# Kernel tuning notes

Hardware: AMD Instinct MI355X
Metric: run time of the kernel (lower is better)

## Reference

```python
import jax, jax.numpy as jnp
import numpy as np

GAMMA_NEG = 4.0
GAMMA_POS = 1.0
CLIP = 0.05
EPS = 1e-08
ALPHA3 = 2.0
TOPK = 10
B, C = 4096, 9605


def setup_inputs() -> dict:
    key = jax.random.key(0)
    k1, k2, k3, k4, k5, k6 = jax.random.split(key, 6)
    x = jax.random.normal(k1, (B, C), dtype=jnp.float32)
    y = (jax.random.uniform(k2, (B, C)) < 0.02).astype(jnp.float32)
    whitelist_mask = jax.random.randint(k3, (C,), 0, 100) == 0
    compost_idx = jax.random.randint(k4, (70,), 0, C, dtype=jnp.int32)
    recycle_idx = jax.random.randint(k5, (70,), 0, C, dtype=jnp.int32)
    donate_idx = jax.random.randint(k6, (70,), 0, C, dtype=jnp.int32)
    return {"x": x, "y": y, "whitelist_mask": whitelist_mask,
            "compost_idx": compost_idx, "recycle_idx": recycle_idx,
            "donate_idx": donate_idx}


def reference(x, y, whitelist_mask, compost_idx, recycle_idx, donate_idx):
    xs_pos = jax.nn.sigmoid(x)                       # [B, C]
    xs_neg = jnp.minimum(1.0 - xs_pos + CLIP, 1.0)   # asymmetric clipping
    # base binary cross-entropy (positive log term, clamped)
    loss = (y * jnp.log(jnp.maximum(xs_pos, EPS))
            + (1.0 - y) * jnp.log(jnp.maximum(xs_neg, EPS)))

    # per-sample: does ground truth hit any whitelist (compost/recycle/donate)?
    wl_idx = jnp.concatenate([compost_idx, recycle_idx, donate_idx])  # [210]
    gt_none = jnp.sum(y[:, wl_idx], axis=1) == 0.0    # [B] -> gt_whitelist == [4]

    # top-10 predictions per sample (argsort descending, first 10)
    _, top10 = jax.lax.top_k(xs_pos, TOPK)            # [B, 10]
    y_top = jnp.take_along_axis(y, top10, axis=1)     # [B, 10]
    wl_top = whitelist_mask[top10]                    # [B, 10]
    # non-whitelisted class: penalize iff gt hits no whitelist
    # whitelisted class:     penalize iff y[i, index] == 0
    penalize = jnp.where(wl_top, y_top == 0.0, gt_none[:, None])  # [B, 10]
    mult_vals = jnp.where(penalize, ALPHA3, 1.0)      # [B, 10]
    rows = jnp.arange(x.shape[0])[:, None]
    mult = jnp.ones_like(loss).at[rows, top10].set(mult_vals)
    loss = loss * mult

    # asymmetric focal weighting (no grad through the weight)
    pt = xs_pos * y + xs_neg * (1.0 - y)
    one_sided_gamma = GAMMA_POS * y + GAMMA_NEG * (1.0 - y)
    one_sided_w = jax.lax.stop_gradient(jnp.power(1.0 - pt, one_sided_gamma))
    loss = loss * one_sided_w
    return -jnp.sum(loss)
```

## Files before the change

### kernel.cpp

```cpp
#include <hip/hip_runtime.h>
#include <stdint.h>

#define B_DIM 4096
#define C_DIM 9605
#define NT 512
#define NW (NT / 64)
#define CHUNKS 4
#define VEC_N (NT * 4 * CHUNKS)
#define TOPK_N 10
#define CAP 1024
#define LOG2E_F 1.4426950408889634f
#define LN2_D 0.6931471805599453
#define CLIP_F 0.05f
#define XTHRESH 2.5f

typedef float f4a __attribute__((ext_vector_type(4), aligned(16)));

__device__ __forceinline__ float sigmoid_f(float x) {
  float e = __builtin_amdgcn_exp2f(-x * LOG2E_F);
  return __builtin_amdgcn_rcpf(1.0f + e);
}

__device__ __forceinline__ float loss2_term(float s, bool pos) {
  float xn = fminf(1.0f + CLIP_F - s, 1.0f);
  float z = pos ? s : xn;
  float logz = __builtin_amdgcn_logf(z);
  float t = fmaxf(s - CLIP_F, 0.0f);
  float t2 = t * t;
  float w = pos ? (1.0f - s) : (t2 * t2);
  return logz * w;
}

__device__ __forceinline__ unsigned long long make_key(float s, int c, bool pos) {
  return ((unsigned long long)__float_as_uint(s) << 15)
       | (unsigned long long)(((uint32_t)(c ^ 0x3FFF) << 1) | (pos ? 1u : 0u));
}

__device__ __forceinline__ void process_elem(float xval, float yval, int c,
                                             float& lsum,
                                             unsigned long long* cand, int* cnt) {
  float s = sigmoid_f(xval);
  bool pos = (yval != 0.0f);
  lsum += loss2_term(s, pos);
  if (xval > XTHRESH) {
    int slot = atomicAdd(cnt, 1);
    if (slot < CAP) cand[slot] = make_key(s, c, pos);
  }
}

__global__ __launch_bounds__(NT, 4) void asym_loss_row_kernel(
    const float* __restrict__ x, const float* __restrict__ y,
    const unsigned char* __restrict__ wl_mask,
    const int* __restrict__ compost, const int* __restrict__ recycle,
    const int* __restrict__ donate, float* __restrict__ row_out) {
  __shared__ unsigned long long cand[CAP];
  __shared__ float s_part[NW];
  __shared__ int s_cnt;
  __shared__ int s_gtany;

  const int row = blockIdx.x;
  const int tid = threadIdx.x;
  const int lane = tid & 63;
  const int wid = tid >> 6;
  const float* xr = x + (size_t)row * C_DIM;
  const float* yr = y + (size_t)row * C_DIM;

  if (tid == 0) { s_cnt = 0; s_gtany = 0; }
  __syncthreads();

  if (tid < 210) {
    int idx = (tid < 70) ? compost[tid]
            : (tid < 140) ? recycle[tid - 70]
                          : donate[tid - 140];
    if (yr[idx] != 0.0f) atomicOr(&s_gtany, 1);
  }

  const int a = (4 - (row & 3)) & 3;
  float lsum = 0.0f;
  if (tid < a) process_elem(xr[tid], yr[tid], tid, lsum, cand, &s_cnt);

  const float* xa = xr + a;
  const float* ya = yr + a;
  f4a X[CHUNKS], Y[CHUNKS];
#pragma unroll
  for (int k = 0; k < CHUNKS; ++k) {
    int c4 = (k * NT + tid) * 4;
    X[k] = *(const f4a*)(xa + c4);
    Y[k] = *(const f4a*)(ya + c4);
  }
#pragma unroll
  for (int k = 0; k < CHUNKS; ++k) {
    int c4 = a + (k * NT + tid) * 4;
#pragma unroll
    for (int j = 0; j < 4; ++j)
      process_elem(X[k][j], Y[k][j], c4 + j, lsum, cand, &s_cnt);
  }
  for (int c = a + VEC_N + tid; c < C_DIM; c += NT)
    process_elem(xr[c], yr[c], c, lsum, cand, &s_cnt);

#pragma unroll
  for (int off = 32; off; off >>= 1) lsum += __shfl_xor(lsum, off, 64);
  if (lane == 0) s_part[wid] = lsum;
  __syncthreads();

  if (wid == 0) {
    const int n = s_cnt;
    const bool gt_none = (s_gtany == 0);
    unsigned long long prev = ~0ull;
    unsigned long long mykey = 0ull;

    if (n >= TOPK_N && n <= CAP) {
#pragma unroll 1
      for (int r = 0; r < TOPK_N; ++r) {
        unsigned long long loc = 0ull;
        for (int i = lane; i < n; i += 64) {
          unsigned long long k = cand[i];
          if (k < prev && k > loc) loc = k;
        }
#pragma unroll
        for (int off = 32; off; off >>= 1) {
          unsigned long long o = __shfl_xor(loc, off, 64);
          loc = loc > o ? loc : o;
        }
        if (lane == r) mykey = loc;
        prev = loc;
      }
    } else {
#pragma unroll 1
      for (int r = 0; r < TOPK_N; ++r) {
        unsigned long long loc = 0ull;
        for (int i = lane; i < C_DIM; i += 64) {
          float s = sigmoid_f(xr[i]);
          unsigned long long k = make_key(s, i, yr[i] != 0.0f);
          if (k < prev && k > loc) loc = k;
        }
#pragma unroll
        for (int off = 32; off; off >>= 1) {
          unsigned long long o = __shfl_xor(loc, off, 64);
          loc = loc > o ? loc : o;
        }
        if (lane == r) mykey = loc;
        prev = loc;
      }
    }

    float extra = 0.0f;
    if (lane < TOPK_N) {
      int wc = 0x3FFF ^ (int)((mykey >> 1) & 0x3FFFull);
      bool ypos = (mykey & 1ull) != 0ull;
      float s = __uint_as_float((uint32_t)(mykey >> 15));
      bool wl = (wl_mask[wc] != 0);
      bool pen = wl ? (!ypos) : gt_none;
      if (pen) extra = loss2_term(s, ypos);
    }
#pragma unroll
    for (int off = 32; off; off >>= 1) extra += __shfl_xor(extra, off, 64);
    if (lane == 0) {
      float tot = extra;
#pragma unroll
      for (int w2 = 0; w2 < NW; ++w2) tot += s_part[w2];
      row_out[row] = tot;
    }
  }
}

__global__ void finalize_kernel(const float* __restrict__ row_out,
                                float* __restrict__ out) {
  const int tid = threadIdx.x;
  const int lane = tid & 63;
  const int wid = tid >> 6;
  __shared__ double sp[4];
  double acc = 0.0;
  for (int i = tid; i < B_DIM; i += 256) acc += (double)row_out[i];
#pragma unroll
  for (int off = 32; off; off >>= 1) acc += __shfl_down(acc, off, 64);
  if (lane == 0) sp[wid] = acc;
  __syncthreads();
  if (tid == 0) {
    double t = sp[0] + sp[1] + sp[2] + sp[3];
    out[0] = (float)(-t * LN2_D);
  }
}

extern "C" void kernel_launch(void* const* d_in, const int* in_sizes, int n_in,
                              void* d_out, int out_size, void* d_ws, size_t ws_size,
                              hipStream_t stream) {
  (void)in_sizes; (void)n_in; (void)out_size; (void)ws_size;
  const float* x = (const float*)d_in[0];
  const float* y = (const float*)d_in[1];
  const unsigned char* wl = (const unsigned char*)d_in[2];
  const int* compost = (const int*)d_in[3];
  const int* recycle = (const int*)d_in[4];
  const int* donate  = (const int*)d_in[5];
  float* row_part = (float*)d_ws;

  asym_loss_row_kernel<<<B_DIM, NT, 0, stream>>>(x, y, wl, compost, recycle,
                                                 donate, row_part);
  finalize_kernel<<<1, 256, 0, stream>>>(row_part, (float*)d_out);
}
```

Measured before the change: 66.15 us.

## Vectorize tail columns, hoist all loads ahead of compute, batch candidate checks

```diff
diff --git a/kernel.cpp b/kernel.cpp
--- a/kernel.cpp
+++ b/kernel.cpp
@@ -5,8 +5,6 @@
 #define C_DIM 9605
 #define NT 512
 #define NW (NT / 64)
-#define CHUNKS 4
-#define VEC_N (NT * 4 * CHUNKS)
 #define TOPK_N 10
 #define CAP 1024
 #define LOG2E_F 1.4426950408889634f
@@ -48,6 +46,27 @@
   }
 }
 
+__device__ __forceinline__ void process4(const f4a xv, const f4a yv, int cb,
+                                         bool active, float& lsum,
+                                         unsigned long long* cand, int* cnt) {
+  float sv[4], l = 0.0f;
+#pragma unroll
+  for (int j = 0; j < 4; ++j) {
+    sv[j] = sigmoid_f(xv[j]);
+    l += loss2_term(sv[j], yv[j] != 0.0f);
+  }
+  if (active) lsum += l;
+  float mx = fmaxf(fmaxf(xv[0], xv[1]), fmaxf(xv[2], xv[3]));
+  if (active && mx > XTHRESH) {
+#pragma unroll
+    for (int j = 0; j < 4; ++j)
+      if (xv[j] > XTHRESH) {
+        int slot = atomicAdd(cnt, 1);
+        if (slot < CAP) cand[slot] = make_key(sv[j], cb + j, yv[j] != 0.0f);
+      }
+  }
+}
+
 __global__ __launch_bounds__(NT, 4) void asym_loss_row_kernel(
     const float* __restrict__ x, const float* __restrict__ y,
     const unsigned char* __restrict__ wl_mask,
@@ -68,34 +87,44 @@
   if (tid == 0) { s_cnt = 0; s_gtany = 0; }
   __syncthreads();
 
+  const int a = (4 - (row & 3)) & 3;
+  const float* xa = xr + a;
+  const float* ya = yr + a;
+  const int Tend = (C_DIM - a - 4) & ~3;
+
+  float ywl = 0.0f;
   if (tid < 210) {
     int idx = (tid < 70) ? compost[tid]
             : (tid < 140) ? recycle[tid - 70]
                           : donate[tid - 140];
-    if (yr[idx] != 0.0f) atomicOr(&s_gtany, 1);
-  }
-
-  const int a = (4 - (row & 3)) & 3;
-  float lsum = 0.0f;
-  if (tid < a) process_elem(xr[tid], yr[tid], tid, lsum, cand, &s_cnt);
-
-  const float* xa = xr + a;
-  const float* ya = yr + a;
-  f4a X[CHUNKS], Y[CHUNKS];
-#pragma unroll
-  for (int k = 0; k < CHUNKS; ++k) {
+    ywl = yr[idx];
+  }
+
+  f4a X[5], Y[5];
+  int c4t = 4 * NT * 4 + 4 * tid;
+  const bool tact = (c4t <= Tend);
+  if (!tact) c4t = Tend;
+#pragma unroll
+  for (int k = 0; k < 4; ++k) {
     int c4 = (k * NT + tid) * 4;
     X[k] = *(const f4a*)(xa + c4);
     Y[k] = *(const f4a*)(ya + c4);
   }
-#pragma unroll
-  for (int k = 0; k < CHUNKS; ++k) {
-    int c4 = a + (k * NT + tid) * 4;
-#pragma unroll
-    for (int j = 0; j < 4; ++j)
-      process_elem(X[k][j], Y[k][j], c4 + j, lsum, cand, &s_cnt);
-  }
-  for (int c = a + VEC_N + tid; c < C_DIM; c += NT)
+  X[4] = *(const f4a*)(xa + c4t);
+  Y[4] = *(const f4a*)(ya + c4t);
+
+  asm volatile("" : "+v"(X[0]), "+v"(X[1]), "+v"(X[2]), "+v"(X[3]), "+v"(X[4]),
+                    "+v"(Y[0]), "+v"(Y[1]), "+v"(Y[2]), "+v"(Y[3]), "+v"(Y[4]));
+
+  if (ywl != 0.0f) atomicOr(&s_gtany, 1);
+
+  float lsum = 0.0f;
+  if (tid < a) process_elem(xr[tid], yr[tid], tid, lsum, cand, &s_cnt);
+#pragma unroll
+  for (int k = 0; k < 4; ++k)
+    process4(X[k], Y[k], a + (k * NT + tid) * 4, true, lsum, cand, &s_cnt);
+  process4(X[4], Y[4], a + c4t, tact, lsum, cand, &s_cnt);
+  for (int c = a + Tend + 4 + tid; c < C_DIM; c += NT)
     process_elem(xr[c], yr[c], c, lsum, cand, &s_cnt);
 
 #pragma unroll
```

After: 63.82 us. 3.5% less time.

## Split row kernel into flat grid-stride stream pass plus per-row top-k kernel

Applied to the files above, without the earlier changes.

```diff
diff --git a/kernel.cpp b/kernel.cpp
--- a/kernel.cpp
+++ b/kernel.cpp
@@ -3,18 +3,22 @@
 
 #define B_DIM 4096
 #define C_DIM 9605
-#define NT 512
-#define NW (NT / 64)
-#define CHUNKS 4
-#define VEC_N (NT * 4 * CHUNKS)
+#define E_TOT 39341965
+#define E_LAST 39341964
+#define QTOT 9835491
+#define NB1 2048
+#define NT1 256
 #define TOPK_N 10
-#define CAP 1024
+#define CAP 80
 #define LOG2E_F 1.4426950408889634f
 #define LN2_D 0.6931471805599453
 #define CLIP_F 0.05f
-#define XTHRESH 2.5f
+#define XTHRESH 2.65f
+#define DIV_MAGIC 114472840ull
+#define DIV_SHIFT 40
 
 typedef float f4a __attribute__((ext_vector_type(4), aligned(16)));
+typedef unsigned long long u64;
 
 __device__ __forceinline__ float sigmoid_f(float x) {
   float e = __builtin_amdgcn_exp2f(-x * LOG2E_F);
@@ -31,147 +35,157 @@
   return logz * w;
 }
 
-__device__ __forceinline__ unsigned long long make_key(float s, int c, bool pos) {
-  return ((unsigned long long)__float_as_uint(s) << 15)
-       | (unsigned long long)(((uint32_t)(c ^ 0x3FFF) << 1) | (pos ? 1u : 0u));
-}
-
-__device__ __forceinline__ void process_elem(float xval, float yval, int c,
-                                             float& lsum,
-                                             unsigned long long* cand, int* cnt) {
-  float s = sigmoid_f(xval);
-  bool pos = (yval != 0.0f);
-  lsum += loss2_term(s, pos);
-  if (xval > XTHRESH) {
-    int slot = atomicAdd(cnt, 1);
-    if (slot < CAP) cand[slot] = make_key(s, c, pos);
-  }
-}
-
-__global__ __launch_bounds__(NT, 4) void asym_loss_row_kernel(
+__device__ __forceinline__ uint32_t fmono(float v) {
+  uint32_t b = __float_as_uint(v);
+  return (b & 0x80000000u) ? ~b : (b | 0x80000000u);
+}
+__device__ __forceinline__ float fmono_dec(uint32_t m) {
+  return __uint_as_float((m & 0x80000000u) ? (m & 0x7FFFFFFFu) : ~m);
+}
+
+__device__ __forceinline__ u64 make_key(float xv, uint32_t col, bool pos) {
+  return ((u64)fmono(xv) << 15)
+       | (u64)(((col ^ 0x3FFFu) << 1) | (pos ? 1u : 0u));
+}
+
+__global__ __launch_bounds__(NT1) void k1_stream(
+    const float* __restrict__ x, const float* __restrict__ y,
+    u64* __restrict__ cand, unsigned int* __restrict__ cnt,
+    float* __restrict__ partial) {
+  const int gtid = blockIdx.x * NT1 + threadIdx.x;
+  float lsum = 0.0f;
+
+  for (int q = gtid; q < QTOT; q += NB1 * NT1) {
+    const uint32_t e = (uint32_t)q * 4u;
+    f4a xv = *(const f4a*)(x + e);
+    f4a yv = *(const f4a*)(y + e);
+#pragma unroll
+    for (int j = 0; j < 4; ++j)
+      lsum += loss2_term(sigmoid_f(xv[j]), yv[j] != 0.0f);
+    float mx = fmaxf(fmaxf(xv[0], xv[1]), fmaxf(xv[2], xv[3]));
+    if (mx > XTHRESH) {
+#pragma unroll
+      for (int j = 0; j < 4; ++j)
+        if (xv[j] > XTHRESH) {
+          uint32_t e4 = e + (uint32_t)j;
+          uint32_t row = (uint32_t)(((u64)e4 * DIV_MAGIC) >> DIV_SHIFT);
+          uint32_t col = e4 - row * (uint32_t)C_DIM;
+          uint32_t slot = atomicAdd(&cnt[row], 1u);
+          if (slot < CAP)
+            cand[(size_t)row * CAP + slot] = make_key(xv[j], col, yv[j] != 0.0f);
+        }
+    }
+  }
+
+  if (gtid == 0) {
+    float xs = x[E_LAST], ys = y[E_LAST];
+    lsum += loss2_term(sigmoid_f(xs), ys != 0.0f);
+    if (xs > XTHRESH) {
+      uint32_t slot = atomicAdd(&cnt[B_DIM - 1], 1u);
+      if (slot < CAP)
+        cand[(size_t)(B_DIM - 1) * CAP + slot] =
+            make_key(xs, (uint32_t)(C_DIM - 1), ys != 0.0f);
+    }
+  }
+
+  const int lane = threadIdx.x & 63;
+  const int wid = threadIdx.x >> 6;
+  __shared__ float sp[NT1 / 64];
+#pragma unroll
+  for (int off = 32; off; off >>= 1) lsum += __shfl_xor(lsum, off, 64);
+  if (lane == 0) sp[wid] = lsum;
+  __syncthreads();
+  if (threadIdx.x == 0) {
+    float t = 0.0f;
+#pragma unroll
+    for (int w = 0; w < NT1 / 64; ++w) t += sp[w];
+    partial[blockIdx.x] = t;
+  }
+}
+
+__global__ __launch_bounds__(64) void k2_topk(
     const float* __restrict__ x, const float* __restrict__ y,
     const unsigned char* __restrict__ wl_mask,
     const int* __restrict__ compost, const int* __restrict__ recycle,
-    const int* __restrict__ donate, float* __restrict__ row_out) {
-  __shared__ unsigned long long cand[CAP];
-  __shared__ float s_part[NW];
-  __shared__ int s_cnt;
-  __shared__ int s_gtany;
-
+    const int* __restrict__ donate,
+    const u64* __restrict__ cand, const unsigned int* __restrict__ cnt,
+    float* __restrict__ extra) {
   const int row = blockIdx.x;
-  const int tid = threadIdx.x;
-  const int lane = tid & 63;
-  const int wid = tid >> 6;
-  const float* xr = x + (size_t)row * C_DIM;
+  const int lane = threadIdx.x;
   const float* yr = y + (size_t)row * C_DIM;
 
-  if (tid == 0) { s_cnt = 0; s_gtany = 0; }
-  __syncthreads();
-
-  if (tid < 210) {
-    int idx = (tid < 70) ? compost[tid]
-            : (tid < 140) ? recycle[tid - 70]
-                          : donate[tid - 140];
-    if (yr[idx] != 0.0f) atomicOr(&s_gtany, 1);
-  }
-
-  const int a = (4 - (row & 3)) & 3;
-  float lsum = 0.0f;
-  if (tid < a) process_elem(xr[tid], yr[tid], tid, lsum, cand, &s_cnt);
-
-  const float* xa = xr + a;
-  const float* ya = yr + a;
-  f4a X[CHUNKS], Y[CHUNKS];
-#pragma unroll
-  for (int k = 0; k < CHUNKS; ++k) {
-    int c4 = (k * NT + tid) * 4;
-    X[k] = *(const f4a*)(xa + c4);
-    Y[k] = *(const f4a*)(ya + c4);
-  }
-#pragma unroll
-  for (int k = 0; k < CHUNKS; ++k) {
-    int c4 = a + (k * NT + tid) * 4;
-#pragma unroll
-    for (int j = 0; j < 4; ++j)
-      process_elem(X[k][j], Y[k][j], c4 + j, lsum, cand, &s_cnt);
-  }
-  for (int c = a + VEC_N + tid; c < C_DIM; c += NT)
-    process_elem(xr[c], yr[c], c, lsum, cand, &s_cnt);
-
-#pragma unroll
-  for (int off = 32; off; off >>= 1) lsum += __shfl_xor(lsum, off, 64);
-  if (lane == 0) s_part[wid] = lsum;
-  __syncthreads();
-
-  if (wid == 0) {
-    const int n = s_cnt;
-    const bool gt_none = (s_gtany == 0);
-    unsigned long long prev = ~0ull;
-    unsigned long long mykey = 0ull;
-
-    if (n >= TOPK_N && n <= CAP) {
+  bool hit = false;
+  for (int i = lane; i < 210; i += 64) {
+    int idx = (i < 70) ? compost[i]
+            : (i < 140) ? recycle[i - 70]
+                        : donate[i - 140];
+    hit |= (yr[idx] != 0.0f);
+  }
+  const bool gt_none = !__any(hit);
+
+  const int n = (int)cnt[row];
+  u64 prev = ~0ull;
+  u64 mykey = 0ull;
+
+  if (n >= TOPK_N && n <= CAP) {
+    const u64* cr = cand + (size_t)row * CAP;
+    u64 k0 = (lane < n) ? cr[lane] : 0ull;
+    u64 k1 = (lane + 64 < n) ? cr[lane + 64] : 0ull;
 #pragma unroll 1
-      for (int r = 0; r < TOPK_N; ++r) {
-        unsigned long long loc = 0ull;
-        for (int i = lane; i < n; i += 64) {
-          unsigned long long k = cand[i];
-          if (k < prev && k > loc) loc = k;
-        }
-#pragma unroll
-        for (int off = 32; off; off >>= 1) {
-          unsigned long long o = __shfl_xor(loc, off, 64);
-          loc = loc > o ? loc : o;
-        }
-        if (lane == r) mykey = loc;
-        prev = loc;
+    for (int r = 0; r < TOPK_N; ++r) {
+      u64 loc = (k0 < prev) ? k0 : 0ull;
+      if (k1 < prev && k1 > loc) loc = k1;
+#pragma unroll
+      for (int off = 32; off; off >>= 1) {
+        u64 o = __shfl_xor(loc, off, 64);
+        loc = loc > o ? loc : o;
       }
-    } else {
+      if (lane == r) mykey = loc;
+      prev = loc;
+    }
+  } else {
+    const float* xr = x + (size_t)row * C_DIM;
 #pragma unroll 1
-      for (int r = 0; r < TOPK_N; ++r) {
-        unsigned long long loc = 0ull;
-        for (int i = lane; i < C_DIM; i += 64) {
-          float s = sigmoid_f(xr[i]);
-          unsigned long long k = make_key(s, i, yr[i] != 0.0f);
-          if (k < prev && k > loc) loc = k;
-        }
-#pragma unroll
-        for (int off = 32; off; off >>= 1) {
-          unsigned long long o = __shfl_xor(loc, off, 64);
-          loc = loc > o ? loc : o;
-        }
-        if (lane == r) mykey = loc;
-        prev = loc;
+    for (int r = 0; r < TOPK_N; ++r) {
+      u64 loc = 0ull;
+      for (int c = lane; c < C_DIM; c += 64) {
+        u64 k = make_key(xr[c], (uint32_t)c, yr[c] != 0.0f);
+        if (k < prev && k > loc) loc = k;
       }
-    }
-
-    float extra = 0.0f;
-    if (lane < TOPK_N) {
-      int wc = 0x3FFF ^ (int)((mykey >> 1) & 0x3FFFull);
-      bool ypos = (mykey & 1ull) != 0ull;
-      float s = __uint_as_float((uint32_t)(mykey >> 15));
-      bool wl = (wl_mask[wc] != 0);
-      bool pen = wl ? (!ypos) : gt_none;
-      if (pen) extra = loss2_term(s, ypos);
-    }
-#pragma unroll
-    for (int off = 32; off; off >>= 1) extra += __shfl_xor(extra, off, 64);
-    if (lane == 0) {
-      float tot = extra;
-#pragma unroll
-      for (int w2 = 0; w2 < NW; ++w2) tot += s_part[w2];
-      row_out[row] = tot;
-    }
-  }
-}
-
-__global__ void finalize_kernel(const float* __restrict__ row_out,
-                                float* __restrict__ out) {
+#pragma unroll
+      for (int off = 32; off; off >>= 1) {
+        u64 o = __shfl_xor(loc, off, 64);
+        loc = loc > o ? loc : o;
+      }
+      if (lane == r) mykey = loc;
+      prev = loc;
+    }
+  }
+
+  float ev = 0.0f;
+  if (lane < TOPK_N) {
+    uint32_t col = 0x3FFFu ^ (uint32_t)((mykey >> 1) & 0x3FFFull);
+    bool yb = (mykey & 1ull) != 0ull;
+    float xv = fmono_dec((uint32_t)(mykey >> 15));
+    bool w = (wl_mask[col] != 0);
+    bool pen = w ? (!yb) : gt_none;
+    if (pen) ev = loss2_term(sigmoid_f(xv), yb);
+  }
+#pragma unroll
+  for (int off = 8; off; off >>= 1) ev += __shfl_down(ev, off, 64);
+  if (lane == 0) extra[row] = ev;
+}
+
+__global__ void k3_finalize(const float* __restrict__ partial,
+                            const float* __restrict__ extra,
+                            float* __restrict__ out) {
   const int tid = threadIdx.x;
   const int lane = tid & 63;
   const int wid = tid >> 6;
   __shared__ double sp[4];
   double acc = 0.0;
-  for (int i = tid; i < B_DIM; i += 256) acc += (double)row_out[i];
+  for (int i = tid; i < NB1; i += 256) acc += (double)partial[i];
+  for (int i = tid; i < B_DIM; i += 256) acc += (double)extra[i];
 #pragma unroll
   for (int off = 32; off; off >>= 1) acc += __shfl_down(acc, off, 64);
   if (lane == 0) sp[wid] = acc;
@@ -192,9 +206,16 @@
   const int* compost = (const int*)d_in[3];
   const int* recycle = (const int*)d_in[4];
   const int* donate  = (const int*)d_in[5];
-  float* row_part = (float*)d_ws;
-
-  asym_loss_row_kernel<<<B_DIM, NT, 0, stream>>>(x, y, wl, compost, recycle,
-                                                 donate, row_part);
-  finalize_kernel<<<1, 256, 0, stream>>>(row_part, (float*)d_out);
-}
+
+  char* ws = (char*)d_ws;
+  u64* cand          = (u64*)ws;
+  unsigned int* cnt  = (unsigned int*)(ws + 2621440);
+  float* partial     = (float*)(ws + 2637824);
+  float* extra       = (float*)(ws + 2646016);
+
+  hipMemsetAsync(cnt, 0, B_DIM * sizeof(unsigned int), stream);
+  k1_stream<<<NB1, NT1, 0, stream>>>(x, y, cand, cnt, partial);
+  k2_topk<<<B_DIM, 64, 0, stream>>>(x, y, wl, compost, recycle, donate,
+                                    cand, cnt, extra);
+  k3_finalize<<<1, 256, 0, stream>>>(partial, extra, (float*)d_out);
+}
```

Result: slower. 116.6 us (+76.2%).
